# Optimization experiments

Measured on AMD Instinct MI355X. Metric: run time of the kernel, lower is better.

Reference implementation:

```python
import math
import jax, jax.numpy as jnp
import numpy as np

B, L, D = 2, 2048, 1024
NH = 16
HS = D // NH
BLOCK_SIZE = 2048


def setup_inputs() -> dict:
    key = jax.random.key(0)
    ks = jax.random.split(key, 4)
    x = jax.random.normal(ks[0], (B, L, D), dtype=jnp.float32)
    Wqkv = jax.random.normal(ks[1], (D, 3 * D), dtype=jnp.float32) * 0.02
    bqkv = jnp.zeros((3 * D,), dtype=jnp.float32)
    Wproj = jax.random.normal(ks[2], (D, D), dtype=jnp.float32) * 0.02
    bproj = jnp.zeros((D,), dtype=jnp.float32)
    Er = jax.random.normal(ks[3], (BLOCK_SIZE, HS), dtype=jnp.float32)
    return {"x": x, "Wqkv": Wqkv, "bqkv": bqkv, "Wproj": Wproj, "bproj": bproj, "Er": Er}


def _skew(QEr):
    # QEr: [B, nh, L, L]  (Music Transformer skew trick)
    b, nh, nr, nc = QEr.shape
    padded = jnp.pad(QEr, ((0, 0), (0, 0), (0, 0), (1, 0)))  # [B, nh, nr, nc+1]
    reshaped = padded.reshape(b, nh, nc + 1, nr)
    return reshaped[:, :, 1:, :]  # [B, nh, nr, nc]


def reference(x, Wqkv, bqkv, Wproj, bproj, Er):
    b, l, d = x.shape
    qkv = x @ Wqkv + bqkv  # [B, L, 3D]
    q, k, v = jnp.split(qkv, 3, axis=2)
    q = q.reshape(b, l, NH, HS).transpose(0, 2, 1, 3)  # [B, nh, L, hs]
    k = k.reshape(b, l, NH, HS).transpose(0, 2, 1, 3)
    v = v.reshape(b, l, NH, HS).transpose(0, 2, 1, 3)

    start = BLOCK_SIZE - l
    Er_t = Er[start:, :].T  # [hs, L]
    QEr = jnp.einsum('bhld,dm->bhlm', q, Er_t)  # [B, nh, L, L]
    Srel = _skew(QEr)

    QK_t = jnp.einsum('bhld,bhmd->bhlm', q, k)
    scale = 1.0 / math.sqrt(HS)
    att = (QK_t + Srel) * scale
    causal = jnp.tril(jnp.ones((l, l), dtype=bool))
    att = jnp.where(causal[None, None, :, :], att, jnp.float32(-jnp.inf))
    att = jax.nn.softmax(att, axis=-1)
    y = jnp.einsum('bhlm,bhmd->bhld', att, v)
    y = y.transpose(0, 2, 1, 3).reshape(b, l, d)
    return y @ Wproj + bproj
```

## Files before the change

kernel.cpp:

```cpp
#include <hip/hip_runtime.h>
#include <stdint.h>

#define BB 2
#define LL 2048
#define DD 1024
#define NHH 16
#define HSS 64

typedef __bf16 bf16x8 __attribute__((ext_vector_type(8)));
typedef float f32x4 __attribute__((ext_vector_type(4)));

__device__ __forceinline__ bf16x8 load8(const float* p) {
  float4 f0 = *(const float4*)p;
  float4 f1 = *(const float4*)(p + 4);
  bf16x8 v;
  v[0] = (__bf16)f0.x; v[1] = (__bf16)f0.y; v[2] = (__bf16)f0.z; v[3] = (__bf16)f0.w;
  v[4] = (__bf16)f1.x; v[5] = (__bf16)f1.y; v[6] = (__bf16)f1.z; v[7] = (__bf16)f1.w;
  return v;
}
__device__ __forceinline__ bf16x8 load8(const __bf16* p) {
  return *(const bf16x8*)p;
}

__device__ __forceinline__ void async_ld16(__bf16* lds_uniform_base,
                                           const __bf16* gptr_per_lane) {
  __builtin_amdgcn_global_load_lds(
      (const __attribute__((address_space(1))) void*)gptr_per_lane,
      (__attribute__((address_space(3))) void*)lds_uniform_base, 16, 0, 0);
}

__global__ void prep_k(const float* __restrict__ Wqkv, const float* __restrict__ x,
                       const float* __restrict__ Er, __bf16* __restrict__ WqkvT,
                       __bf16* __restrict__ xb, __bf16* __restrict__ Erb) {
  int tx = threadIdx.x, ty = threadIdx.y;
  int tid = ty * 32 + tx;
  if (blockIdx.z == 1) {
    if (blockIdx.x >= 2048) return;
    size_t off = ((size_t)blockIdx.x * 256 + tid) * 8;
    *(bf16x8*)&xb[off] = load8(&x[off]);
    return;
  }
  if (blockIdx.z == 2) {
    if (blockIdx.x >= 64) return;
    size_t off = ((size_t)blockIdx.x * 256 + tid) * 8;
    *(bf16x8*)&Erb[off] = load8(&Er[off]);
    return;
  }
  __shared__ __bf16 tile[32][33];
  int c0 = (blockIdx.x % 96) * 32, r0 = (blockIdx.x / 96) * 32;
#pragma unroll
  for (int i = ty; i < 32; i += 8)
    tile[i][tx] = (__bf16)Wqkv[(size_t)(r0 + i) * 3072 + c0 + tx];
  __syncthreads();
#pragma unroll
  for (int i = ty; i < 32; i += 8)
    WqkvT[(size_t)(c0 + i) * 1024 + r0 + tx] = tile[tx][i];
}

__global__ __launch_bounds__(256) void gemm_qkv_k(
    const __bf16* __restrict__ A, const __bf16* __restrict__ Bt,
    const float* __restrict__ bias, __bf16* __restrict__ Qo,
    __bf16* __restrict__ Ko, __bf16* __restrict__ Vto) {
  const int K = 1024;
  __shared__ __align__(16) __bf16 smem[4 * 4096];
  __bf16* Vl = smem;
  int t = threadIdx.x;
  int wave = t >> 6, lane = t & 63, qd = lane >> 4, lr = lane & 15;
  int wg = (int)blockIdx.y * 24 + (int)blockIdx.x;
  wg = (wg & 7) * 96 + (wg >> 3);
  int m0 = (wg / 24) * 128, n0 = (wg % 24) * 128;
  int wm = (wave >> 1) * 64, wn = (wave & 1) * 64;
  f32x4 acc[4][4] = {};
  int srow = lane >> 2, sch = (lane & 3) * 8;
  const __bf16* Ab[2];
  const __bf16* Bb[2];
#pragma unroll
  for (int c = 0; c < 2; c++) {
    Ab[c] = A + (size_t)(m0 + (wave * 2 + c) * 16 + srow) * K + sch;
    Bb[c] = Bt + (size_t)(n0 + (wave * 2 + c) * 16 + srow) * K + sch;
  }
#pragma unroll
  for (int c = 0; c < 2; c++) {
    async_ld16(&smem[0 * 4096 + (wave * 2 + c) * 512], Ab[c]);
    async_ld16(&smem[2 * 4096 + (wave * 2 + c) * 512], Bb[c]);
  }
  __syncthreads();
  int cur = 0;
  for (int k0 = 0; k0 < K; k0 += 32) {
    if (k0 + 32 < K) {
#pragma unroll
      for (int c = 0; c < 2; c++) {
        async_ld16(&smem[(cur ^ 1) * 4096 + (wave * 2 + c) * 512], Ab[c] + k0 + 32);
        async_ld16(&smem[(2 + (cur ^ 1)) * 4096 + (wave * 2 + c) * 512], Bb[c] + k0 + 32);
      }
    }
    const __bf16* As = &smem[cur * 4096];
    const __bf16* Bs = &smem[(2 + cur) * 4096];
    bf16x8 af[4], bfr[4];
#pragma unroll
    for (int mt = 0; mt < 4; mt++)
      af[mt] = *(const bf16x8*)&As[(wm + mt * 16 + lr) * 32 + qd * 8];
#pragma unroll
    for (int nt = 0; nt < 4; nt++)
      bfr[nt] = *(const bf16x8*)&Bs[(wn + nt * 16 + lr) * 32 + qd * 8];
#pragma unroll
    for (int mt = 0; mt < 4; mt++)
#pragma unroll
      for (int nt = 0; nt < 4; nt++)
        acc[mt][nt] = __builtin_amdgcn_mfma_f32_16x16x32_bf16(af[mt], bfr[nt],
                                                              acc[mt][nt], 0, 0, 0);
    __syncthreads();
    cur ^= 1;
  }
  float bvv[4];
#pragma unroll
  for (int nt = 0; nt < 4; nt++) bvv[nt] = bias[n0 + wn + nt * 16 + lr];

  if (n0 < 2 * DD) {
#pragma unroll
    for (int mt = 0; mt < 4; mt++)
#pragma unroll
      for (int nt = 0; nt < 4; nt++)
#pragma unroll
        for (int r = 0; r < 4; r++) {
          int row = m0 + wm + mt * 16 + qd * 4 + r;
          int col = n0 + wn + nt * 16 + lr;
          __bf16 bb = (__bf16)(acc[mt][nt][r] + bvv[nt]);
          int b = row >> 11, l = row & 2047;
          int h = (col >> 6) & 15, d = col & 63;
          if (col < DD) {
            Qo[(((size_t)(b * NHH + h)) * LL + l) * HSS + d] = bb;
          } else {
            Ko[(((size_t)(b * NHH + h)) * LL + l) * HSS + d] = bb;
          }
        }
  } else {
    int vb0 = n0 - 2 * DD;
    int bq = m0 >> 11, l0 = m0 & 2047;
    int vr = t >> 2, vc = (t & 3) * 8;
#pragma unroll
    for (int c = 0; c < 2; c++) {
      if ((wave & 1) == c) {
#pragma unroll
        for (int mt = 0; mt < 4; mt++)
#pragma unroll
          for (int nt = 0; nt < 4; nt++)
#pragma unroll
            for (int r = 0; r < 4; r++) {
              int vrow = nt * 16 + lr;
              int ml = wm + mt * 16 + qd * 4 + r;
              Vl[vrow * 136 + ml] = (__bf16)(acc[mt][nt][r] + bvv[nt]);
            }
      }
      __syncthreads();
      int h = (vb0 + c * 64) >> 6;
      __bf16* dst = Vto + (((size_t)(bq * NHH + h)) * HSS + vr) * LL + l0 + vc;
      const __bf16* src = &Vl[vr * 136 + vc];
#pragma unroll
      for (int u = 0; u < 4; u++)
        *(bf16x8*)(dst + u * 32) = *(const bf16x8*)(src + u * 32);
      __syncthreads();
    }
  }
}

__global__ __launch_bounds__(256) void gemm_proj_k(
    const __bf16* __restrict__ A, const __bf16* __restrict__ Bt,
    const float* __restrict__ bias, float* __restrict__ out) {
  const int K = 1024, N = 1024;
  __shared__ __align__(16) __bf16 smem[2 * 4096 + 2 * 2048];
  int t = threadIdx.x;
  int wave = t >> 6, lane = t & 63, qd = lane >> 4, lr = lane & 15;
  int wg = (int)blockIdx.y * 16 + (int)blockIdx.x;
  wg = (wg & 7) * 64 + (wg >> 3);
  int m0 = (wg / 16) * 128, n0 = (wg % 16) * 64;
  int wm = (wave >> 1) * 64, wn = (wave & 1) * 32;
  f32x4 acc[4][2] = {};
  int srow = lane >> 2, sch = (lane & 3) * 8;
  const __bf16* Ab[2];
  const __bf16* Bb;
#pragma unroll
  for (int c = 0; c < 2; c++)
    Ab[c] = A + (size_t)(m0 + (wave * 2 + c) * 16 + srow) * K + sch;
  Bb = Bt + (size_t)(n0 + wave * 16 + srow) * K + sch;

#pragma unroll
  for (int c = 0; c < 2; c++)
    async_ld16(&smem[0 * 4096 + (wave * 2 + c) * 512], Ab[c]);
  async_ld16(&smem[2 * 4096 + wave * 512], Bb);
  __syncthreads();
  int cur = 0;
  for (int k0 = 0; k0 < K; k0 += 32) {
    if (k0 + 32 < K) {
#pragma unroll
      for (int c = 0; c < 2; c++)
        async_ld16(&smem[(cur ^ 1) * 4096 + (wave * 2 + c) * 512], Ab[c] + k0 + 32);
      async_ld16(&smem[2 * 4096 + (cur ^ 1) * 2048 + wave * 512], Bb + k0 + 32);
    }
    const __bf16* As = &smem[cur * 4096];
    const __bf16* Bs = &smem[2 * 4096 + cur * 2048];
    bf16x8 af[4], bfr[2];
#pragma unroll
    for (int mt = 0; mt < 4; mt++)
      af[mt] = *(const bf16x8*)&As[(wm + mt * 16 + lr) * 32 + qd * 8];
#pragma unroll
    for (int nt = 0; nt < 2; nt++)
      bfr[nt] = *(const bf16x8*)&Bs[(wn + nt * 16 + lr) * 32 + qd * 8];
#pragma unroll
    for (int mt = 0; mt < 4; mt++)
#pragma unroll
      for (int nt = 0; nt < 2; nt++)
        acc[mt][nt] = __builtin_amdgcn_mfma_f32_16x16x32_bf16(af[mt], bfr[nt],
                                                              acc[mt][nt], 0, 0, 0);
    __syncthreads();
    cur ^= 1;
  }
  float bvv[2];
#pragma unroll
  for (int nt = 0; nt < 2; nt++) bvv[nt] = bias[n0 + wn + nt * 16 + lr];
#pragma unroll
  for (int mt = 0; mt < 4; mt++)
#pragma unroll
    for (int nt = 0; nt < 2; nt++)
#pragma unroll
      for (int r = 0; r < 4; r++) {
        int row = m0 + wm + mt * 16 + qd * 4 + r;
        int col = n0 + wn + nt * 16 + lr;
        out[(size_t)row * N + col] = acc[mt][nt][r] + bvv[nt];
      }
}

__global__ __launch_bounds__(256, 3) void flash_k(
    const __bf16* __restrict__ Qg, const __bf16* __restrict__ Kg,
    const __bf16* __restrict__ Vtg, const __bf16* __restrict__ Erb,
    __bf16* __restrict__ Po0, __bf16* __restrict__ Po1,
    float* __restrict__ Lp0, float* __restrict__ Lp1) {
  __shared__ __align__(16) __bf16 Kbuf[2][64 * 64];
  __shared__ __align__(16) __bf16 Vbuf[2][64 * 64];
  __shared__ __align__(16) __bf16 Pball[4][16 * 64];

  int bh = blockIdx.x;
  int tile = 31 - (int)blockIdx.y;
  int i0 = tile * 64;
  int niter = tile + 1;
  int mid = (niter + 1) >> 1;
  int it0 = (blockIdx.z == 0) ? 0 : mid;
  int it1 = (blockIdx.z == 0) ? mid : niter;
  const __bf16* Qh = Qg + (size_t)bh * LL * HSS;
  const __bf16* Kh = Kg + (size_t)bh * LL * HSS;
  const __bf16* Vth = Vtg + (size_t)bh * HSS * LL;
  int b = bh >> 4, h = bh & 15;
  int t = threadIdx.x, wave = t >> 6, lane = t & 63, qd = lane >> 4, lr = lane & 15;
  __bf16* Pb = &Pball[wave][0];
  int cbase = 48 - wave * 16;

  const float SC = 0.18033688011112042f;

  int lrow = lane >> 3;
  int lcol = ((lane & 7) ^ lrow) * 8;
  const __bf16* KsrcB[2];
  const __bf16* VsrcB[2];
#pragma unroll
  for (int c = 0; c < 2; c++) {
    int q = wave * 2 + c;
    KsrcB[c] = Kh + (size_t)(q * 8 + lrow) * HSS + lcol;
    VsrcB[c] = Vth + (size_t)(q * 8 + lrow) * LL + lcol;
  }

  int swA = (qd ^ (lr & 7)) * 8;
  int swB = ((qd + 4) ^ (lr & 7)) * 8;

  int hi8 = lr >> 3;
  int ib0 = 15 - qd * 4 + lr;
  int pb0 = qd * 256 + (lr & 7);
  int px0 = (qd & 1) * 4;
  int rowb = i0 + wave * 16 + qd * 4;

  bf16x8 aq[2];
  {
    const __bf16* qrow = Qh + (size_t)(i0 + wave * 16 + lr) * HSS + qd * 8;
    aq[0] = *(const bf16x8*)qrow;
    aq[1] = *(const bf16x8*)(qrow + 32);
  }
  f32x4 oacc[4] = {};
  float lsum[4] = {};

  int cur = 0;
  if (it0 < it1) {
    int j0 = it0 * 64;
#pragma unroll
    for (int c = 0; c < 2; c++) {
      async_ld16(&Kbuf[0][(wave * 2 + c) * 512], KsrcB[c] + (size_t)j0 * HSS);
      async_ld16(&Vbuf[0][(wave * 2 + c) * 512], VsrcB[c] + j0);
    }
  }
  __syncthreads();

  for (int it = it0; it < it1; ++it) {
    int j0 = it * 64;

    if (it + 1 < it1) {
      int jn = (it + 1) * 64;
#pragma unroll
      for (int c = 0; c < 2; c++) {
        async_ld16(&Kbuf[cur ^ 1][(wave * 2 + c) * 512], KsrcB[c] + (size_t)jn * HSS);
        async_ld16(&Vbuf[cur ^ 1][(wave * 2 + c) * 512], VsrcB[c] + jn);
      }
    }

    int ebase = LL - 64 - i0 + j0 + cbase + lr;
    int e[5];
#pragma unroll
    for (int ct = 0; ct < 5; ct++) {
      int v = ebase + ct * 16;
      e[ct] = (v < LL) ? v : (LL - 1);
    }
    bf16x8 ef0[5];
#pragma unroll
    for (int ct = 0; ct < 5; ct++)
      ef0[ct] = *(const bf16x8*)&Erb[(size_t)e[ct] * HSS + qd * 8];

    const __bf16* Kb = &Kbuf[cur][0];
    const __bf16* Vb = &Vbuf[cur][0];

    f32x4 sacc[4] = {};
    __builtin_amdgcn_s_setprio(1);
#pragma unroll
    for (int ct = 0; ct < 4; ct++) {
      bf16x8 bk0 = *(const bf16x8*)&Kb[(ct * 16 + lr) * 64 + swA];
      bf16x8 bk1 = *(const bf16x8*)&Kb[(ct * 16 + lr) * 64 + swB];
      sacc[ct] = __builtin_amdgcn_mfma_f32_16x16x32_bf16(aq[0], bk0, sacc[ct], 0, 0, 0);
      sacc[ct] = __builtin_amdgcn_mfma_f32_16x16x32_bf16(aq[1], bk1, sacc[ct], 0, 0, 0);
    }
    __builtin_amdgcn_s_setprio(0);

    bf16x8 ef1[5];
#pragma unroll
    for (int ct = 0; ct < 5; ct++)
      ef1[ct] = *(const bf16x8*)&Erb[(size_t)e[ct] * HSS + 32 + qd * 8];

    f32x4 racc[5] = {};
    __builtin_amdgcn_s_setprio(1);
#pragma unroll
    for (int ct = 0; ct < 5; ct++)
      racc[ct] = __builtin_amdgcn_mfma_f32_16x16x32_bf16(aq[0], ef0[ct], racc[ct], 0, 0, 0);
#pragma unroll
    for (int ct = 0; ct < 5; ct++)
      racc[ct] = __builtin_amdgcn_mfma_f32_16x16x32_bf16(aq[1], ef1[ct], racc[ct], 0, 0, 0);
    __builtin_amdgcn_s_setprio(0);

    int dib = rowb - j0;
#pragma unroll
    for (int r = 0; r < 4; r++) {
      int bse = ib0 - r;
      int hi = bse >> 4;
      int idx = (qd * 16 + (bse & 15)) << 2;
      float sh[5];
#pragma unroll
      for (int ct = 0; ct < 5; ct++)
        sh[ct] = __int_as_float(
            __builtin_amdgcn_ds_bpermute(idx, __float_as_int(racc[ct][r])));
      int di = dib + r;
#pragma unroll
      for (int ct2 = 0; ct2 < 4; ct2++) {
        float rel = hi ? sh[ct2 + 1] : sh[ct2];
        float p = __builtin_exp2f((sacc[ct2][r] + rel) * SC);
        p = (ct2 * 16 + lr <= di) ? p : 0.f;
        __bf16 pb = (__bf16)p;
        lsum[r] += (float)pb;
        Pb[pb0 + r * 64 + (((2 * ct2 + hi8) ^ (px0 + r)) << 3)] = pb;
      }
    }

    bf16x8 ap0 = *(const bf16x8*)&Pb[lr * 64 + swA];
    bf16x8 ap1 = *(const bf16x8*)&Pb[lr * 64 + swB];
    __builtin_amdgcn_s_setprio(1);
#pragma unroll
    for (int dt = 0; dt < 4; dt++) {
      bf16x8 bv0 = *(const bf16x8*)&Vb[(dt * 16 + lr) * 64 + swA];
      bf16x8 bv1 = *(const bf16x8*)&Vb[(dt * 16 + lr) * 64 + swB];
      oacc[dt] = __builtin_amdgcn_mfma_f32_16x16x32_bf16(ap0, bv0, oacc[dt], 0, 0, 0);
      oacc[dt] = __builtin_amdgcn_mfma_f32_16x16x32_bf16(ap1, bv1, oacc[dt], 0, 0, 0);
    }
    __builtin_amdgcn_s_setprio(0);

    __syncthreads();
    cur ^= 1;
  }

#pragma unroll
  for (int r = 0; r < 4; r++) {
#pragma unroll
    for (int m = 1; m < 16; m <<= 1)
      lsum[r] += __shfl_xor(lsum[r], m, 64);
  }

  __bf16* Po = (blockIdx.z == 0) ? Po0 : Po1;
  float* Lp = (blockIdx.z == 0) ? Lp0 : Lp1;
#pragma unroll
  for (int r = 0; r < 4; r++) {
    int l = i0 + wave * 16 + qd * 4 + r;
    if (lr == 0) Lp[(size_t)bh * LL + l] = lsum[r];
#pragma unroll
    for (int dt = 0; dt < 4; dt++) {
      int d = dt * 16 + lr;
      Po[((size_t)(b * LL) + l) * DD + h * HSS + d] = (__bf16)oacc[dt][r];
    }
  }
}

__global__ void ct_k(const __bf16* __restrict__ Po0,
                     const __bf16* __restrict__ Po1,
                     const float* __restrict__ Lp0,
                     const float* __restrict__ Lp1,
                     __bf16* __restrict__ Y,
                     const float* __restrict__ Wproj,
                     __bf16* __restrict__ WprojT) {
  int id = blockIdx.x;
  if (id < 2048) {
    size_t f = ((size_t)id * 256 + threadIdx.x) * 8;
    int dfull = (int)(f & 1023);
    int h = dfull >> 6;
    int l = (int)((f >> 10) & 2047);
    int b = (int)(f >> 21);
    size_t lidx = ((size_t)(b * NHH + h)) * LL + l;
    float linv = 1.f / (Lp0[lidx] + Lp1[lidx]);
    bf16x8 a = *(const bf16x8*)&Po0[f];
    bf16x8 c = *(const bf16x8*)&Po1[f];
    bf16x8 o;
#pragma unroll
    for (int q = 0; q < 8; q++)
      o[q] = (__bf16)(((float)a[q] + (float)c[q]) * linv);
    *(bf16x8*)&Y[f] = o;
    return;
  }
  __shared__ __bf16 tile[32][33];
  int q = id - 2048;
  int c0 = (q & 31) * 32, r0 = (q >> 5) * 32;
  int tx = threadIdx.x & 31, ty = threadIdx.x >> 5;
#pragma unroll
  for (int i = ty; i < 32; i += 8)
    tile[i][tx] = (__bf16)Wproj[(size_t)(r0 + i) * 1024 + c0 + tx];
  __syncthreads();
#pragma unroll
  for (int i = ty; i < 32; i += 8)
    WprojT[(size_t)(c0 + i) * 1024 + r0 + tx] = tile[tx][i];
}

extern "C" void kernel_launch(void* const* d_in, const int* in_sizes, int n_in,
                              void* d_out, int out_size, void* d_ws, size_t ws_size,
                              hipStream_t stream) {
  const float* x = (const float*)d_in[0];
  const float* Wqkv = (const float*)d_in[1];
  const float* bqkv = (const float*)d_in[2];
  const float* Wproj = (const float*)d_in[3];
  const float* bproj = (const float*)d_in[4];
  const float* Er = (const float*)d_in[5];
  float* out = (float*)d_out;

  if (ws_size < 4u * 8388608u) return;

  uint8_t* w = (uint8_t*)d_ws;
  __bf16* Q = (__bf16*)w;  w += (size_t)BB * NHH * LL * HSS * 2;
  __bf16* Kt = (__bf16*)w; w += (size_t)BB * NHH * LL * HSS * 2;
  __bf16* Vt = (__bf16*)w; w += (size_t)BB * NHH * LL * HSS * 2;
  __bf16* Y = (__bf16*)w;  w += (size_t)BB * LL * DD * 2;

  __bf16* WqkvT = (__bf16*)d_out;
  __bf16* xb = (__bf16*)((uint8_t*)d_out + (size_t)3072 * 1024 * 2);
  __bf16* Erb = (__bf16*)((uint8_t*)d_out + (size_t)3072 * 1024 * 2 + (size_t)4096 * 1024 * 2);
  __bf16* Po1 = (__bf16*)d_out;
  float* Lp0 = (float*)((uint8_t*)d_out + (size_t)BB * LL * DD * 2);
  float* Lp1 = (float*)((uint8_t*)d_out + (size_t)BB * LL * DD * 2 + (size_t)BB * NHH * LL * 4);
  __bf16* Po0 = Y;
  __bf16* WprojT = Q;

  prep_k<<<dim3(3072, 1, 3), dim3(32, 8), 0, stream>>>(Wqkv, x, Er, WqkvT, xb, Erb);
  gemm_qkv_k<<<dim3(3072 / 128, 4096 / 128), 256, 0, stream>>>(
      xb, WqkvT, bqkv, Q, Kt, Vt);
  flash_k<<<dim3(BB * NHH, 32, 2), 256, 0, stream>>>(
      Q, Kt, Vt, Erb, Po0, Po1, Lp0, Lp1);
  ct_k<<<dim3(3072), 256, 0, stream>>>(Po0, Po1, Lp0, Lp1, Y, Wproj, WprojT);
  gemm_proj_k<<<dim3(1024 / 64, 4096 / 128), 256, 0, stream>>>(Y, WprojT, bproj, out);
}
```

Before: 236.0 us.

## Triple-buffer LDS tiles in QKV and projection GEMMs with partial vmcnt waits

Both GEMM kernels switch from double-buffered to triple-buffered async global-to-LDS loads. Each iteration prefetches two K-tiles ahead and uses a manual s_waitcnt vmcnt(N) plus s_barrier instead of a full __syncthreads. The intent is to keep more loads in flight so memory latency is hidden behind the MFMA work. In exchange the kernels use more LDS, which may reduce occupancy. The tail iterations also issue redundant loads of the last tile.

```diff
diff --git a/kernel.cpp b/kernel.cpp
--- a/kernel.cpp
+++ b/kernel.cpp
@@ -62,7 +62,7 @@
     const float* __restrict__ bias, __bf16* __restrict__ Qo,
     __bf16* __restrict__ Ko, __bf16* __restrict__ Vto) {
   const int K = 1024;
-  __shared__ __align__(16) __bf16 smem[4 * 4096];
+  __shared__ __align__(16) __bf16 smem[6 * 4096];
   __bf16* Vl = smem;
   int t = threadIdx.x;
   int wave = t >> 6, lane = t & 63, qd = lane >> 4, lr = lane & 15;
@@ -80,22 +80,29 @@
     Bb[c] = Bt + (size_t)(n0 + (wave * 2 + c) * 16 + srow) * K + sch;
   }
 #pragma unroll
-  for (int c = 0; c < 2; c++) {
-    async_ld16(&smem[0 * 4096 + (wave * 2 + c) * 512], Ab[c]);
-    async_ld16(&smem[2 * 4096 + (wave * 2 + c) * 512], Bb[c]);
-  }
-  __syncthreads();
-  int cur = 0;
-  for (int k0 = 0; k0 < K; k0 += 32) {
-    if (k0 + 32 < K) {
-#pragma unroll
-      for (int c = 0; c < 2; c++) {
-        async_ld16(&smem[(cur ^ 1) * 4096 + (wave * 2 + c) * 512], Ab[c] + k0 + 32);
-        async_ld16(&smem[(2 + (cur ^ 1)) * 4096 + (wave * 2 + c) * 512], Bb[c] + k0 + 32);
-      }
-    }
-    const __bf16* As = &smem[cur * 4096];
-    const __bf16* Bs = &smem[(2 + cur) * 4096];
+  for (int kt = 0; kt < 2; kt++) {
+#pragma unroll
+    for (int c = 0; c < 2; c++) {
+      async_ld16(&smem[kt * 4096 + (wave * 2 + c) * 512], Ab[c] + kt * 32);
+      async_ld16(&smem[(3 + kt) * 4096 + (wave * 2 + c) * 512], Bb[c] + kt * 32);
+    }
+  }
+  asm volatile("s_waitcnt vmcnt(4)" ::: "memory");
+  __builtin_amdgcn_s_barrier();
+  __builtin_amdgcn_sched_barrier(0);
+
+  for (int kt = 0; kt < 32; kt++) {
+    int ktn = kt + 2;
+    int bi = ktn % 3;
+    int k0n = ((ktn < 32) ? ktn : 31) * 32;
+#pragma unroll
+    for (int c = 0; c < 2; c++) {
+      async_ld16(&smem[bi * 4096 + (wave * 2 + c) * 512], Ab[c] + k0n);
+      async_ld16(&smem[(3 + bi) * 4096 + (wave * 2 + c) * 512], Bb[c] + k0n);
+    }
+    int rb = kt % 3;
+    const __bf16* As = &smem[rb * 4096];
+    const __bf16* Bs = &smem[(3 + rb) * 4096];
     bf16x8 af[4], bfr[4];
 #pragma unroll
     for (int mt = 0; mt < 4; mt++)
@@ -109,9 +116,13 @@
       for (int nt = 0; nt < 4; nt++)
         acc[mt][nt] = __builtin_amdgcn_mfma_f32_16x16x32_bf16(af[mt], bfr[nt],
                                                               acc[mt][nt], 0, 0, 0);
-    __syncthreads();
-    cur ^= 1;
-  }
+    asm volatile("s_waitcnt vmcnt(4)" ::: "memory");
+    __builtin_amdgcn_s_barrier();
+    __builtin_amdgcn_sched_barrier(0);
+  }
+  asm volatile("s_waitcnt vmcnt(0)" ::: "memory");
+  __syncthreads();
+
   float bvv[4];
 #pragma unroll
   for (int nt = 0; nt < 4; nt++) bvv[nt] = bias[n0 + wn + nt * 16 + lr];
@@ -168,7 +179,7 @@
     const __bf16* __restrict__ A, const __bf16* __restrict__ Bt,
     const float* __restrict__ bias, float* __restrict__ out) {
   const int K = 1024, N = 1024;
-  __shared__ __align__(16) __bf16 smem[2 * 4096 + 2 * 2048];
+  __shared__ __align__(16) __bf16 smem[3 * 4096 + 3 * 2048];
   int t = threadIdx.x;
   int wave = t >> 6, lane = t & 63, qd = lane >> 4, lr = lane & 15;
   int wg = (int)blockIdx.y * 16 + (int)blockIdx.x;
@@ -185,20 +196,27 @@
   Bb = Bt + (size_t)(n0 + wave * 16 + srow) * K + sch;
 
 #pragma unroll
-  for (int c = 0; c < 2; c++)
-    async_ld16(&smem[0 * 4096 + (wave * 2 + c) * 512], Ab[c]);
-  async_ld16(&smem[2 * 4096 + wave * 512], Bb);
-  __syncthreads();
-  int cur = 0;
-  for (int k0 = 0; k0 < K; k0 += 32) {
-    if (k0 + 32 < K) {
-#pragma unroll
-      for (int c = 0; c < 2; c++)
-        async_ld16(&smem[(cur ^ 1) * 4096 + (wave * 2 + c) * 512], Ab[c] + k0 + 32);
-      async_ld16(&smem[2 * 4096 + (cur ^ 1) * 2048 + wave * 512], Bb + k0 + 32);
-    }
-    const __bf16* As = &smem[cur * 4096];
-    const __bf16* Bs = &smem[2 * 4096 + cur * 2048];
+  for (int kt = 0; kt < 2; kt++) {
+#pragma unroll
+    for (int c = 0; c < 2; c++)
+      async_ld16(&smem[kt * 4096 + (wave * 2 + c) * 512], Ab[c] + kt * 32);
+    async_ld16(&smem[3 * 4096 + kt * 2048 + wave * 512], Bb + kt * 32);
+  }
+  asm volatile("s_waitcnt vmcnt(3)" ::: "memory");
+  __builtin_amdgcn_s_barrier();
+  __builtin_amdgcn_sched_barrier(0);
+
+  for (int kt = 0; kt < 32; kt++) {
+    int ktn = kt + 2;
+    int bi = ktn % 3;
+    int k0n = ((ktn < 32) ? ktn : 31) * 32;
+#pragma unroll
+    for (int c = 0; c < 2; c++)
+      async_ld16(&smem[bi * 4096 + (wave * 2 + c) * 512], Ab[c] + k0n);
+    async_ld16(&smem[3 * 4096 + bi * 2048 + wave * 512], Bb + k0n);
+    int rb = kt % 3;
+    const __bf16* As = &smem[rb * 4096];
+    const __bf16* Bs = &smem[3 * 4096 + rb * 2048];
     bf16x8 af[4], bfr[2];
 #pragma unroll
     for (int mt = 0; mt < 4; mt++)
@@ -212,8 +230,9 @@
       for (int nt = 0; nt < 2; nt++)
         acc[mt][nt] = __builtin_amdgcn_mfma_f32_16x16x32_bf16(af[mt], bfr[nt],
                                                               acc[mt][nt], 0, 0, 0);
-    __syncthreads();
-    cur ^= 1;
+    asm volatile("s_waitcnt vmcnt(3)" ::: "memory");
+    __builtin_amdgcn_s_barrier();
+    __builtin_amdgcn_sched_barrier(0);
   }
   float bvv[2];
 #pragma unroll
```

Measured after the change: 238.0 us. About the same (+0.9%).

## Rewrite QKV GEMM with 256x256 tiles, 8 waves, swizzled LDS and interleaved pipeline

Applied to the files above, without the earlier changes.

The QKV projection GEMM moves from 128x128 tiles with 4 waves to 256x256 tiles with 8 waves and K-steps of 64. It adds XOR-swizzled LDS layouts to avoid bank conflicts, splits loads into phases interleaved with MFMA groups, and uses s_setprio raised during MFMA bursts. The aim is more reuse per loaded byte and better overlap of global loads with matrix math. The cost is that the grid shrinks to 192 workgroups, which may underfill the GPU's compute units, and 128 KB of LDS limits how many workgroups fit per CU.

```diff
diff --git a/kernel.cpp b/kernel.cpp
--- a/kernel.cpp
+++ b/kernel.cpp
@@ -57,74 +57,162 @@
     WqkvT[(size_t)(c0 + i) * 1024 + r0 + tx] = tile[tx][i];
 }
 
-__global__ __launch_bounds__(256) void gemm_qkv_k(
+__global__ __launch_bounds__(512, 2) void gemm_qkv_k(
     const __bf16* __restrict__ A, const __bf16* __restrict__ Bt,
     const float* __restrict__ bias, __bf16* __restrict__ Qo,
     __bf16* __restrict__ Ko, __bf16* __restrict__ Vto) {
-  const int K = 1024;
-  __shared__ __align__(16) __bf16 smem[4 * 4096];
-  __bf16* Vl = smem;
+  __shared__ __align__(16) __bf16 smem[65536];
   int t = threadIdx.x;
   int wave = t >> 6, lane = t & 63, qd = lane >> 4, lr = lane & 15;
-  int wg = (int)blockIdx.y * 24 + (int)blockIdx.x;
-  wg = (wg & 7) * 96 + (wg >> 3);
-  int m0 = (wg / 24) * 128, n0 = (wg % 24) * 128;
-  int wm = (wave >> 1) * 64, wn = (wave & 1) * 64;
-  f32x4 acc[4][4] = {};
-  int srow = lane >> 2, sch = (lane & 3) * 8;
-  const __bf16* Ab[2];
-  const __bf16* Bb[2];
-#pragma unroll
-  for (int c = 0; c < 2; c++) {
-    Ab[c] = A + (size_t)(m0 + (wave * 2 + c) * 16 + srow) * K + sch;
-    Bb[c] = Bt + (size_t)(n0 + (wave * 2 + c) * 16 + srow) * K + sch;
-  }
-#pragma unroll
-  for (int c = 0; c < 2; c++) {
-    async_ld16(&smem[0 * 4096 + (wave * 2 + c) * 512], Ab[c]);
-    async_ld16(&smem[2 * 4096 + (wave * 2 + c) * 512], Bb[c]);
-  }
+  int wr = wave >> 2, wc = wave & 3;
+  int wg = (int)blockIdx.x;
+  wg = (wg & 7) * 24 + (wg >> 3);
+  int m0 = (wg / 12) * 256, n0 = (wg % 12) * 256;
+
+  int lrow = lane >> 3, lchk = ((lane & 7) ^ lrow) * 8;
+  const __bf16* Abase = A + (size_t)(m0 + wave * 16 + lrow) * 1024 + lchk;
+  const __bf16* Bbase = Bt + (size_t)(n0 + wave * 16 + lrow) * 1024 + lchk;
+
+  int swk0 = (qd ^ (lr & 7)) * 8;
+  int swk1 = ((4 + qd) ^ (lr & 7)) * 8;
+
+  f32x4 acc[8][4] = {};
+  bf16x8 af[4][2], bf[4][2];
+
+#define STAGE_A(slot, kt)                                                      \
+  {                                                                            \
+    int ko_ = (kt) * 64;                                                       \
+    async_ld16(&smem[(slot) * 16384 + (wave * 16) * 64], Abase + ko_);         \
+    async_ld16(&smem[(slot) * 16384 + (wave * 16 + 8) * 64],                   \
+               Abase + 8 * 1024 + ko_);                                        \
+    async_ld16(&smem[(slot) * 16384 + (128 + wave * 16) * 64],                 \
+               Abase + 128 * 1024 + ko_);                                      \
+    async_ld16(&smem[(slot) * 16384 + (136 + wave * 16) * 64],                 \
+               Abase + 136 * 1024 + ko_);                                      \
+  }
+#define STAGE_B(slot, kt)                                                      \
+  {                                                                            \
+    int ko_ = (kt) * 64;                                                       \
+    async_ld16(&smem[32768 + (slot) * 16384 + (wave * 16) * 64], Bbase + ko_); \
+    async_ld16(&smem[32768 + (slot) * 16384 + (wave * 16 + 8) * 64],           \
+               Bbase + 8 * 1024 + ko_);                                        \
+    async_ld16(&smem[32768 + (slot) * 16384 + (128 + wave * 16) * 64],         \
+               Bbase + 128 * 1024 + ko_);                                      \
+    async_ld16(&smem[32768 + (slot) * 16384 + (136 + wave * 16) * 64],         \
+               Bbase + 136 * 1024 + ko_);                                      \
+  }
+#define LDA(slot, mt, kc)                                                      \
+  (*(const bf16x8*)&smem[(slot) * 16384 + (wr * 128 + (mt) * 16 + lr) * 64 +   \
+                         ((kc) ? swk1 : swk0)])
+#define LDB(slot, nt, kc)                                                      \
+  (*(const bf16x8*)&smem[32768 + (slot) * 16384 +                              \
+                         (wc * 64 + (nt) * 16 + lr) * 64 +                     \
+                         ((kc) ? swk1 : swk0)])
+
+  STAGE_A(0, 0);
+  STAGE_B(0, 0);
+  asm volatile("s_waitcnt vmcnt(0)" ::: "memory");
   __syncthreads();
-  int cur = 0;
-  for (int k0 = 0; k0 < K; k0 += 32) {
-    if (k0 + 32 < K) {
-#pragma unroll
-      for (int c = 0; c < 2; c++) {
-        async_ld16(&smem[(cur ^ 1) * 4096 + (wave * 2 + c) * 512], Ab[c] + k0 + 32);
-        async_ld16(&smem[(2 + (cur ^ 1)) * 4096 + (wave * 2 + c) * 512], Bb[c] + k0 + 32);
-      }
-    }
-    const __bf16* As = &smem[cur * 4096];
-    const __bf16* Bs = &smem[(2 + cur) * 4096];
-    bf16x8 af[4], bfr[4];
+
+  for (int kt = 0; kt < 16; kt++) {
+    int s = kt & 1, sn = s ^ 1;
+    int ktn = (kt < 15) ? kt + 1 : 15;
+
+#pragma unroll
+    for (int mt = 0; mt < 4; mt++) {
+      af[mt][0] = LDA(s, mt, 0);
+      af[mt][1] = LDA(s, mt, 1);
+    }
+#pragma unroll
+    for (int nt = 0; nt < 2; nt++) {
+      bf[nt][0] = LDB(s, nt, 0);
+      bf[nt][1] = LDB(s, nt, 1);
+    }
+    STAGE_A(sn, ktn);
+    __builtin_amdgcn_s_barrier();
+    asm volatile("s_waitcnt lgkmcnt(0)" ::: "memory");
+    __builtin_amdgcn_sched_barrier(0);
+    __builtin_amdgcn_s_setprio(1);
 #pragma unroll
     for (int mt = 0; mt < 4; mt++)
-      af[mt] = *(const bf16x8*)&As[(wm + mt * 16 + lr) * 32 + qd * 8];
-#pragma unroll
-    for (int nt = 0; nt < 4; nt++)
-      bfr[nt] = *(const bf16x8*)&Bs[(wn + nt * 16 + lr) * 32 + qd * 8];
+#pragma unroll
+      for (int nt = 0; nt < 2; nt++) {
+        acc[mt][nt] = __builtin_amdgcn_mfma_f32_16x16x32_bf16(af[mt][0], bf[nt][0], acc[mt][nt], 0, 0, 0);
+        acc[mt][nt] = __builtin_amdgcn_mfma_f32_16x16x32_bf16(af[mt][1], bf[nt][1], acc[mt][nt], 0, 0, 0);
+      }
+    __builtin_amdgcn_s_setprio(0);
+    __builtin_amdgcn_s_barrier();
+
+#pragma unroll
+    for (int nt = 2; nt < 4; nt++) {
+      bf[nt][0] = LDB(s, nt, 0);
+      bf[nt][1] = LDB(s, nt, 1);
+    }
+    STAGE_B(sn, ktn);
+    __builtin_amdgcn_s_barrier();
+    asm volatile("s_waitcnt lgkmcnt(0)" ::: "memory");
+    __builtin_amdgcn_sched_barrier(0);
+    __builtin_amdgcn_s_setprio(1);
 #pragma unroll
     for (int mt = 0; mt < 4; mt++)
 #pragma unroll
+      for (int nt = 2; nt < 4; nt++) {
+        acc[mt][nt] = __builtin_amdgcn_mfma_f32_16x16x32_bf16(af[mt][0], bf[nt][0], acc[mt][nt], 0, 0, 0);
+        acc[mt][nt] = __builtin_amdgcn_mfma_f32_16x16x32_bf16(af[mt][1], bf[nt][1], acc[mt][nt], 0, 0, 0);
+      }
+    __builtin_amdgcn_s_setprio(0);
+    __builtin_amdgcn_s_barrier();
+
+#pragma unroll
+    for (int mt = 0; mt < 4; mt++) {
+      af[mt][0] = LDA(s, mt + 4, 0);
+      af[mt][1] = LDA(s, mt + 4, 1);
+    }
+    __builtin_amdgcn_s_barrier();
+    asm volatile("s_waitcnt lgkmcnt(0)" ::: "memory");
+    __builtin_amdgcn_sched_barrier(0);
+    __builtin_amdgcn_s_setprio(1);
+#pragma unroll
+    for (int mt = 0; mt < 4; mt++)
+#pragma unroll
+      for (int nt = 0; nt < 2; nt++) {
+        acc[mt + 4][nt] = __builtin_amdgcn_mfma_f32_16x16x32_bf16(af[mt][0], bf[nt][0], acc[mt + 4][nt], 0, 0, 0);
+        acc[mt + 4][nt] = __builtin_amdgcn_mfma_f32_16x16x32_bf16(af[mt][1], bf[nt][1], acc[mt + 4][nt], 0, 0, 0);
+      }
+    __builtin_amdgcn_s_setprio(0);
+    __builtin_amdgcn_s_barrier();
+
+    __builtin_amdgcn_s_setprio(1);
+#pragma unroll
+    for (int mt = 0; mt < 4; mt++)
+#pragma unroll
+      for (int nt = 2; nt < 4; nt++) {
+        acc[mt + 4][nt] = __builtin_amdgcn_mfma_f32_16x16x32_bf16(af[mt][0], bf[nt][0], acc[mt + 4][nt], 0, 0, 0);
+        acc[mt + 4][nt] = __builtin_amdgcn_mfma_f32_16x16x32_bf16(af[mt][1], bf[nt][1], acc[mt + 4][nt], 0, 0, 0);
+      }
+    __builtin_amdgcn_s_setprio(0);
+    asm volatile("s_waitcnt vmcnt(0)" ::: "memory");
+    __builtin_amdgcn_s_barrier();
+  }
+#undef STAGE_A
+#undef STAGE_B
+#undef LDA
+#undef LDB
+
+  float bvv[4];
+#pragma unroll
+  for (int nt = 0; nt < 4; nt++) bvv[nt] = bias[n0 + wc * 64 + nt * 16 + lr];
+
+  int bq = m0 >> 11, l0 = m0 & 2047;
+  if (n0 < 2 * DD) {
+#pragma unroll
+    for (int mt = 0; mt < 8; mt++)
+#pragma unroll
       for (int nt = 0; nt < 4; nt++)
-        acc[mt][nt] = __builtin_amdgcn_mfma_f32_16x16x32_bf16(af[mt], bfr[nt],
-                                                              acc[mt][nt], 0, 0, 0);
-    __syncthreads();
-    cur ^= 1;
-  }
-  float bvv[4];
-#pragma unroll
-  for (int nt = 0; nt < 4; nt++) bvv[nt] = bias[n0 + wn + nt * 16 + lr];
-
-  if (n0 < 2 * DD) {
-#pragma unroll
-    for (int mt = 0; mt < 4; mt++)
-#pragma unroll
-      for (int nt = 0; nt < 4; nt++)
 #pragma unroll
         for (int r = 0; r < 4; r++) {
-          int row = m0 + wm + mt * 16 + qd * 4 + r;
-          int col = n0 + wn + nt * 16 + lr;
+          int row = m0 + wr * 128 + mt * 16 + qd * 4 + r;
+          int col = n0 + wc * 64 + nt * 16 + lr;
           __bf16 bb = (__bf16)(acc[mt][nt][r] + bvv[nt]);
           int b = row >> 11, l = row & 2047;
           int h = (col >> 6) & 15, d = col & 63;
@@ -135,30 +223,30 @@
           }
         }
   } else {
+    __bf16* Vl = smem;
     int vb0 = n0 - 2 * DD;
-    int bq = m0 >> 11, l0 = m0 & 2047;
-    int vr = t >> 2, vc = (t & 3) * 8;
-#pragma unroll
-    for (int c = 0; c < 2; c++) {
-      if ((wave & 1) == c) {
-#pragma unroll
-        for (int mt = 0; mt < 4; mt++)
+    int vr = t >> 3, vc = (t & 7) * 32;
+#pragma unroll
+    for (int c = 0; c < 4; c++) {
+      if (wc == c) {
+#pragma unroll
+        for (int mt = 0; mt < 8; mt++)
 #pragma unroll
           for (int nt = 0; nt < 4; nt++)
 #pragma unroll
             for (int r = 0; r < 4; r++) {
-              int vrow = nt * 16 + lr;
-              int ml = wm + mt * 16 + qd * 4 + r;
-              Vl[vrow * 136 + ml] = (__bf16)(acc[mt][nt][r] + bvv[nt]);
+              int d = nt * 16 + lr;
+              int ml = wr * 128 + mt * 16 + qd * 4 + r;
+              Vl[d * 264 + ml] = (__bf16)(acc[mt][nt][r] + bvv[nt]);
             }
       }
       __syncthreads();
       int h = (vb0 + c * 64) >> 6;
       __bf16* dst = Vto + (((size_t)(bq * NHH + h)) * HSS + vr) * LL + l0 + vc;
-      const __bf16* src = &Vl[vr * 136 + vc];
+      const __bf16* src = &Vl[vr * 264 + vc];
 #pragma unroll
       for (int u = 0; u < 4; u++)
-        *(bf16x8*)(dst + u * 32) = *(const bf16x8*)(src + u * 32);
+        *(bf16x8*)(dst + u * 8) = *(const bf16x8*)(src + u * 8);
       __syncthreads();
     }
   }
@@ -476,8 +564,7 @@
   __bf16* WprojT = Q;
 
   prep_k<<<dim3(3072, 1, 3), dim3(32, 8), 0, stream>>>(Wqkv, x, Er, WqkvT, xb, Erb);
-  gemm_qkv_k<<<dim3(3072 / 128, 4096 / 128), 256, 0, stream>>>(
-      xb, WqkvT, bqkv, Q, Kt, Vt);
+  gemm_qkv_k<<<dim3(192), 512, 0, stream>>>(xb, WqkvT, bqkv, Q, Kt, Vt);
   flash_k<<<dim3(BB * NHH, 32, 2), 256, 0, stream>>>(
       Q, Kt, Vt, Erb, Po0, Po1, Lp0, Lp1);
   ct_k<<<dim3(3072), 256, 0, stream>>>(Po0, Po1, Lp0, Lp1, Y, Wproj, WprojT);
```

After: 240.9 us. 1.02x slower.
